# Kernel tuning notes

Measured on AMD Instinct MI355X. Metric: run time of the kernel, lower is better.

The kernel has to match this reference:

```python
import jax, jax.numpy as jnp
import numpy as np

B, T, D, H = 2, 2048, 1024, 16
DH = D // H


def setup_inputs() -> dict:
    key = jax.random.key(0)
    ks = jax.random.split(key, 11)
    s = 1.0 / np.sqrt(D)
    return {
        "q": jax.random.normal(ks[0], (B, T, D), jnp.float32),
        "k": jax.random.normal(ks[1], (B, T, D), jnp.float32),
        "v": jax.random.normal(ks[2], (B, T, D), jnp.float32),
        "wq_w": jax.random.normal(ks[3], (D, D), jnp.float32) * s,
        "wq_b": jnp.zeros((D,), jnp.float32),
        "wk_w": jax.random.normal(ks[4], (D, D), jnp.float32) * s,
        "wk_b": jnp.zeros((D,), jnp.float32),
        "wv_w": jax.random.normal(ks[5], (D, D), jnp.float32) * s,
        "wv_b": jnp.zeros((D,), jnp.float32),
        "wo_w": jax.random.normal(ks[6], (D, D), jnp.float32) * s,
        "wo_b": jnp.zeros((D,), jnp.float32),
    }


def reference(q, k, v, wq_w, wq_b, wk_w, wk_b, wv_w, wv_b, wo_w, wo_b):
    b, t, d = q.shape
    # Linear projections (torch Linear: x @ W^T + b)
    wq = (q @ wq_w.T + wq_b).reshape(b, t, H, DH)
    wk = (k @ wk_w.T + wk_b).reshape(b, t, H, DH)
    wv = (v @ wv_w.T + wv_b).reshape(b, t, H, DH)
    # scaled dot-product attention: [b,h,t,s]
    scores = jnp.einsum('bthd,bshd->bhts', wq, wk) / jnp.sqrt(jnp.float32(DH))
    probs = jax.nn.softmax(scores, axis=-1)
    attn = jnp.einsum('bhts,bshd->bthd', probs, wv)  # [b,t,h,dh]
    attn = attn.reshape(b, t, d)
    return attn @ wo_w.T + wo_b
```

## Files before the change

kernel.cpp:

```cpp
#include <hip/hip_runtime.h>
#include <hip/hip_bf16.h>
#include <stdint.h>

#define Bn  2
#define Tn  2048
#define Dn  1024
#define Hn  16
#define DHn 64
#define Mn  (Bn*Tn)

typedef __attribute__((ext_vector_type(8))) short short8;
typedef __attribute__((ext_vector_type(4))) short short4v;
typedef __attribute__((ext_vector_type(4))) float f32x4;

__device__ __forceinline__ f32x4 fzero4() { f32x4 z = {0.f, 0.f, 0.f, 0.f}; return z; }

#define TR16(dst, a32) asm volatile("ds_read_b64_tr_b16 %0, %1" : "=v"(dst) : "v"(a32))

__global__ void cvt4_kernel(const float* __restrict__ a0, const float* __restrict__ a1,
                            const float* __restrict__ a2, const float* __restrict__ a3,
                            __hip_bfloat16* __restrict__ o0, __hip_bfloat16* __restrict__ o1,
                            __hip_bfloat16* __restrict__ o2, __hip_bfloat16* __restrict__ o3, int n)
{
    const int i = (blockIdx.x * blockDim.x + threadIdx.x) * 8;
    if (i >= n) return;
    const float* in = blockIdx.y == 0 ? a0 : (blockIdx.y == 1 ? a1 : (blockIdx.y == 2 ? a2 : a3));
    __hip_bfloat16* out = blockIdx.y == 0 ? o0 : (blockIdx.y == 1 ? o1 : (blockIdx.y == 2 ? o2 : o3));
    float4 a = *(const float4*)(in + i);
    float4 b = *(const float4*)(in + i + 4);
    union { __hip_bfloat16 h[8]; short8 u; } tmp;
    tmp.h[0] = __float2bfloat16(a.x); tmp.h[1] = __float2bfloat16(a.y);
    tmp.h[2] = __float2bfloat16(a.z); tmp.h[3] = __float2bfloat16(a.w);
    tmp.h[4] = __float2bfloat16(b.x); tmp.h[5] = __float2bfloat16(b.y);
    tmp.h[6] = __float2bfloat16(b.z); tmp.h[7] = __float2bfloat16(b.w);
    *(short8*)(out + i) = tmp.u;
}

__global__ __launch_bounds__(256, 2)
void gemm_qkv_kernel(const float* __restrict__ qa, const float* __restrict__ ka,
                     const float* __restrict__ va,
                     const __hip_bfloat16* __restrict__ wq, const __hip_bfloat16* __restrict__ wk,
                     const __hip_bfloat16* __restrict__ wv,
                     const float* __restrict__ bq_, const float* __restrict__ bk_,
                     const float* __restrict__ bv_,
                     __hip_bfloat16* __restrict__ Qp, __hip_bfloat16* __restrict__ Kp,
                     __hip_bfloat16* __restrict__ Vp)
{
    __shared__ alignas(16) short As[2][128*32];
    __shared__ alignas(16) short Bs[2][128*32];
    const int grp = blockIdx.y >> 3;
    const float* A           = grp == 0 ? qa : (grp == 1 ? ka : va);
    const __hip_bfloat16* Bw = grp == 0 ? wq : (grp == 1 ? wk : wv);
    const float* bias        = grp == 0 ? bq_ : (grp == 1 ? bk_ : bv_);
    __hip_bfloat16* C        = grp == 0 ? Qp : (grp == 1 ? Kp : Vp);

    const int t = threadIdx.x, lane = t & 63, wave = t >> 6;
    const int wm = wave >> 1, wn = wave & 1;
    const int row0 = blockIdx.x * 128, col0 = (blockIdx.y & 7) * 128;

    f32x4 acc[4][4];
#pragma unroll
    for (int m = 0; m < 4; ++m)
#pragma unroll
        for (int n = 0; n < 4; ++n) acc[m][n] = fzero4();

    const int srow = wave*16 + (lane >> 2);
    const int skk  = (lane & 3) * 8;
    const int ldsb = wave * 1024 + (lane & 63) * 16;

    float4 ra[2][2];
    auto LOAD_A = [&](int k0) {
#pragma unroll
        for (int i = 0; i < 2; ++i) {
            const float* ap = A + (size_t)(row0 + i*64 + srow)*Dn + k0 + skk;
            ra[i][0] = *(const float4*)ap;
            ra[i][1] = *(const float4*)(ap + 4);
        }
    };
    auto WRITE_A = [&](int buf) {
#pragma unroll
        for (int i = 0; i < 2; ++i) {
            union { __hip_bfloat16 h[8]; short8 u; } w;
            w.h[0] = __float2bfloat16(ra[i][0].x); w.h[1] = __float2bfloat16(ra[i][0].y);
            w.h[2] = __float2bfloat16(ra[i][0].z); w.h[3] = __float2bfloat16(ra[i][0].w);
            w.h[4] = __float2bfloat16(ra[i][1].x); w.h[5] = __float2bfloat16(ra[i][1].y);
            w.h[6] = __float2bfloat16(ra[i][1].z); w.h[7] = __float2bfloat16(ra[i][1].w);
            *(short8*)((char*)As[buf] + i*4096 + ldsb) = w.u;
        }
    };
    auto STAGE_B = [&](int buf, int k0) {
#pragma unroll
        for (int i = 0; i < 2; ++i)
            __builtin_amdgcn_global_load_lds(
                (const __attribute__((address_space(1))) void*)(Bw + (size_t)(col0 + i*64 + srow)*Dn + k0 + skk),
                (__attribute__((address_space(3))) void*)((char*)Bs[buf] + i*4096 + wave*1024 + (lane&63)*16), 16, 0, 0);
    };

    LOAD_A(0);
    STAGE_B(0, 0);
    WRITE_A(0);
    __syncthreads();
    int cur = 0;
    for (int k0 = 0; k0 < Dn; k0 += 32) {
        const bool more = (k0 + 32 < Dn);
        if (more) { LOAD_A(k0 + 32); STAGE_B(cur ^ 1, k0 + 32); }
        short8 af[4], bf_[4];
#pragma unroll
        for (int m = 0; m < 4; ++m)
            af[m] = *(const short8*)((char*)As[cur] + (wm*64 + m*16 + (lane & 15))*64 + (lane >> 4)*16);
#pragma unroll
        for (int n = 0; n < 4; ++n)
            bf_[n] = *(const short8*)((char*)Bs[cur] + (wn*64 + n*16 + (lane & 15))*64 + (lane >> 4)*16);
        __builtin_amdgcn_s_setprio(1);
#pragma unroll
        for (int m = 0; m < 4; ++m)
#pragma unroll
            for (int n = 0; n < 4; ++n)
                acc[m][n] = __builtin_amdgcn_mfma_f32_16x16x32_bf16(af[m], bf_[n], acc[m][n], 0, 0, 0);
        __builtin_amdgcn_s_setprio(0);
        __builtin_amdgcn_sched_barrier(0);
        if (more) WRITE_A(cur ^ 1);
        __syncthreads();
        cur ^= 1;
    }

#pragma unroll
    for (int n = 0; n < 4; ++n) {
        const int col = col0 + wn*64 + n*16 + (lane & 15);
        const float bv = bias[col];
#pragma unroll
        for (int m = 0; m < 4; ++m) {
            const int rb_ = row0 + wm*64 + m*16 + (lane>>4)*4;
#pragma unroll
            for (int i = 0; i < 4; ++i)
                C[(size_t)(rb_+i)*Dn + col] = __float2bfloat16(acc[m][n][i] + bv);
        }
    }
}

__global__ __launch_bounds__(256, 2)
void gemm_out_kernel(const __hip_bfloat16* __restrict__ A,
                     const __hip_bfloat16* __restrict__ Bw,
                     const float* __restrict__ bias,
                     float* __restrict__ C)
{
    __shared__ alignas(16) short As[2][64*32];
    __shared__ alignas(16) short Bs[2][128*32];
    const int t = threadIdx.x, lane = t & 63, wave = t >> 6;
    const int wm = wave >> 1, wn = wave & 1;
    const int row0 = blockIdx.x * 64, col0 = blockIdx.y * 128;

    f32x4 acc[2][4];
#pragma unroll
    for (int m = 0; m < 2; ++m)
#pragma unroll
        for (int n = 0; n < 4; ++n) acc[m][n] = fzero4();

    const int srow = wave*16 + (lane >> 2);
    const int skk  = (lane & 3) * 8;
    const int ldsb = wave * 1024;

    auto STAGE = [&](int buf, int k0) {
        __builtin_amdgcn_global_load_lds(
            (const __attribute__((address_space(1))) void*)(A + (size_t)(row0 + srow)*Dn + k0 + skk),
            (__attribute__((address_space(3))) void*)((char*)As[buf] + ldsb), 16, 0, 0);
#pragma unroll
        for (int i = 0; i < 2; ++i)
            __builtin_amdgcn_global_load_lds(
                (const __attribute__((address_space(1))) void*)(Bw + (size_t)(col0 + i*64 + srow)*Dn + k0 + skk),
                (__attribute__((address_space(3))) void*)((char*)Bs[buf] + i*4096 + ldsb), 16, 0, 0);
    };

    STAGE(0, 0);
    __syncthreads();
    int cur = 0;
    for (int k0 = 0; k0 < Dn; k0 += 32) {
        if (k0 + 32 < Dn) STAGE(cur ^ 1, k0 + 32);
        short8 af[2], bf_[4];
#pragma unroll
        for (int m = 0; m < 2; ++m)
            af[m] = *(const short8*)((char*)As[cur] + (wm*32 + m*16 + (lane & 15))*64 + (lane >> 4)*16);
#pragma unroll
        for (int n = 0; n < 4; ++n)
            bf_[n] = *(const short8*)((char*)Bs[cur] + (wn*64 + n*16 + (lane & 15))*64 + (lane >> 4)*16);
        __builtin_amdgcn_s_setprio(1);
#pragma unroll
        for (int m = 0; m < 2; ++m)
#pragma unroll
            for (int n = 0; n < 4; ++n)
                acc[m][n] = __builtin_amdgcn_mfma_f32_16x16x32_bf16(af[m], bf_[n], acc[m][n], 0, 0, 0);
        __builtin_amdgcn_s_setprio(0);
        __syncthreads();
        cur ^= 1;
    }

#pragma unroll
    for (int n = 0; n < 4; ++n) {
        const int col = col0 + wn*64 + n*16 + (lane & 15);
        const float bv = bias[col];
#pragma unroll
        for (int m = 0; m < 2; ++m) {
            const int rb_ = row0 + wm*32 + m*16 + (lane>>4)*4;
#pragma unroll
            for (int i = 0; i < 4; ++i)
                C[(size_t)(rb_+i)*Dn + col] = acc[m][n][i] + bv;
        }
    }
}

#define VPL 1288

__global__ __launch_bounds__(256, 2)
void attn_kernel(const __hip_bfloat16* __restrict__ Q,
                 const __hip_bfloat16* __restrict__ K,
                 const __hip_bfloat16* __restrict__ V,
                 __hip_bfloat16* __restrict__ O)
{
    __shared__ alignas(16) short Vlds[2*2*4*VPL];
    const int t = threadIdx.x, lane = t & 63, wave = t >> 6;
    const int g = lane >> 4, c = lane & 15;
    const int pk = wave & 1, qh = wave >> 1;
    const int blk = (blockIdx.x & 7) * 64 + (blockIdx.x >> 3);
    const int qb = blk & 15;
    const int h  = (blk >> 4) & (Hn - 1);
    const int b  = blk >> 8;
    const size_t base = (size_t)b * Tn * Dn + (size_t)h * DHn;
    const int q0 = qb * 128 + qh * 64;
    const float cexp = 0.18033688011112042f;

    short8 bq[4][2];
#pragma unroll
    for (int qs = 0; qs < 4; ++qs) {
        const __hip_bfloat16* qp = Q + base + (size_t)(q0 + qs*16 + c) * Dn + g*8;
        bq[qs][0] = *(const short8*)qp;
        bq[qs][1] = *(const short8*)(qp + 32);
    }
    short8 ones;
#pragma unroll
    for (int i = 0; i < 8; ++i) ones[i] = (short)0x3F80;

    f32x4 o_[4][4];
#pragma unroll
    for (int qs = 0; qs < 4; ++qs)
#pragma unroll
        for (int d = 0; d < 4; ++d) o_[qs][d] = fzero4();
    float m_[4] = {-3e38f, -3e38f, -3e38f, -3e38f};
    f32x4 lacc[4] = {fzero4(), fzero4(), fzero4(), fzero4()};

    const int vrow = t >> 3;
    const int vd0  = ((t>>1)&3)*VPL + (vrow>>2)*80 + (vrow&3)*16 + (t&1)*8;
    const int vcol = (((t>>1)&3)*16 + (t&1)*8);
    const uint32_t vbase = (uint32_t)(uintptr_t)(void*)Vlds;
    const uint32_t atr = vbase + (uint32_t)(pk*10304 + g*160 + c*8);

    short8 akA[4][2], akB[4][2];
    {
        const __hip_bfloat16* kp = K + base + (size_t)(pk*64 + c) * Dn + g*8;
#pragma unroll
        for (int sub = 0; sub < 4; ++sub)
#pragma unroll
            for (int ks = 0; ks < 2; ++ks)
                akA[sub][ks] = *(const short8*)(kp + (size_t)sub*16*Dn + ks*32);
    }

    auto ITER = [&](const short8 (&ck)[4][2], short8 (&nk)[4][2], int it) {
        const int kv0 = it * 128;
        short8 cv[2][2];
#pragma unroll
        for (int p = 0; p < 2; ++p) {
            const __hip_bfloat16* vp = V + base + (size_t)(kv0 + p*64 + vrow) * Dn + vcol;
            cv[p][0] = *(const short8*)vp;
            cv[p][1] = *(const short8*)(vp + (size_t)32*Dn);
        }
        {
            const int kvn = (it < 15) ? kv0 + 128 + pk*64 : pk*64;
            const __hip_bfloat16* kp = K + base + (size_t)(kvn + c) * Dn + g*8;
#pragma unroll
            for (int sub = 0; sub < 4; ++sub)
#pragma unroll
                for (int ks = 0; ks < 2; ++ks)
                    nk[sub][ks] = *(const short8*)(kp + (size_t)sub*16*Dn + ks*32);
        }

        short8 pa[4][2];
#pragma unroll
        for (int qs = 0; qs < 4; ++qs) {
            f32x4 s_[4];
#pragma unroll
            for (int sub = 0; sub < 4; ++sub) s_[sub] = fzero4();
            __builtin_amdgcn_s_setprio(1);
#pragma unroll
            for (int sub = 0; sub < 4; ++sub)
#pragma unroll
                for (int ks = 0; ks < 2; ++ks)
                    s_[sub] = __builtin_amdgcn_mfma_f32_16x16x32_bf16(
                        ck[sub][ks], bq[qs][ks], s_[sub], 0, 0, 0);
            __builtin_amdgcn_s_setprio(0);

            float rm = s_[0][0];
#pragma unroll
            for (int sub = 0; sub < 4; ++sub)
#pragma unroll
                for (int i = 0; i < 4; ++i) rm = fmaxf(rm, s_[sub][i]);
            if (!__all((rm - m_[qs]) * cexp <= 8.0f)) {
                float gm = fmaxf(rm, __shfl_xor(rm, 16));
                gm = fmaxf(gm, __shfl_xor(gm, 32));
                const float mn = fmaxf(m_[qs], gm);
                const float sc = exp2f((m_[qs] - mn) * cexp);
                m_[qs] = mn;
#pragma unroll
                for (int i = 0; i < 4; ++i) lacc[qs][i] *= sc;
#pragma unroll
                for (int d = 0; d < 4; ++d)
#pragma unroll
                    for (int i = 0; i < 4; ++i) o_[qs][d][i] *= sc;
            }
            const float mn = m_[qs];
#pragma unroll
            for (int kc = 0; kc < 2; ++kc)
#pragma unroll
                for (int hf = 0; hf < 2; ++hf)
#pragma unroll
                    for (int i = 0; i < 4; ++i) {
                        const float p = exp2f((s_[kc*2+hf][i] - mn) * cexp);
                        union { __hip_bfloat16 hb; short u; } cvp;
                        cvp.hb = __float2bfloat16(p);
                        pa[qs][kc][hf*4 + i] = cvp.u;
                    }
            lacc[qs] = __builtin_amdgcn_mfma_f32_16x16x32_bf16(ones, pa[qs][0], lacc[qs], 0, 0, 0);
            lacc[qs] = __builtin_amdgcn_mfma_f32_16x16x32_bf16(ones, pa[qs][1], lacc[qs], 0, 0, 0);
        }

        short* vb = Vlds + (it & 1) * 10304;
#pragma unroll
        for (int p = 0; p < 2; ++p) {
            *(short8*)(vb + p*5152 + vd0)       = cv[p][0];
            *(short8*)(vb + p*5152 + vd0 + 640) = cv[p][1];
        }
        asm volatile("s_waitcnt lgkmcnt(0)" ::: "memory");
        __builtin_amdgcn_s_barrier();
        __builtin_amdgcn_sched_barrier(0);

        const uint32_t atrb = atr + (uint32_t)((it & 1) * 20608u);
        short4v tv[4][2][2];
#pragma unroll
        for (int d = 0; d < 4; ++d)
#pragma unroll
            for (int kc = 0; kc < 2; ++kc) {
                const uint32_t a = atrb + (uint32_t)(d*2576 + kc*1280);
                TR16(tv[d][kc][0], a);
                TR16(tv[d][kc][1], a + 640);
            }
#pragma unroll
        for (int d = 0; d < 4; ++d) {
            if (d == 0)      asm volatile("s_waitcnt lgkmcnt(12)" ::: "memory");
            else if (d == 1) asm volatile("s_waitcnt lgkmcnt(8)" ::: "memory");
            else if (d == 2) asm volatile("s_waitcnt lgkmcnt(4)" ::: "memory");
            else             asm volatile("s_waitcnt lgkmcnt(0)" ::: "memory");
            __builtin_amdgcn_sched_barrier(0);
            const short8 av0 = __builtin_shufflevector(tv[d][0][0], tv[d][0][1], 0,1,2,3,4,5,6,7);
            const short8 av1 = __builtin_shufflevector(tv[d][1][0], tv[d][1][1], 0,1,2,3,4,5,6,7);
            __builtin_amdgcn_s_setprio(1);
#pragma unroll
            for (int qs = 0; qs < 4; ++qs) {
                o_[qs][d] = __builtin_amdgcn_mfma_f32_16x16x32_bf16(av0, pa[qs][0], o_[qs][d], 0, 0, 0);
                o_[qs][d] = __builtin_amdgcn_mfma_f32_16x16x32_bf16(av1, pa[qs][1], o_[qs][d], 0, 0, 0);
            }
            __builtin_amdgcn_s_setprio(0);
        }
    };

    for (int j = 0; j < 8; ++j) {
        ITER(akA, akB, 2*j);
        ITER(akB, akA, 2*j + 1);
    }

    __syncthreads();
    float* cbase = (float*)Vlds;
    if (pk == 1) {
        float* cb = cbase + qh * 4608;
#pragma unroll
        for (int qs = 0; qs < 4; ++qs)
#pragma unroll
            for (int d = 0; d < 4; ++d)
                *(f32x4*)(cb + ((qs*4 + d)*64 + lane)*4) = o_[qs][d];
#pragma unroll
        for (int qs = 0; qs < 4; ++qs) {
            cb[4096 + qs*64 + lane] = m_[qs];
            cb[4352 + qs*64 + lane] = lacc[qs][0];
        }
    }
    __syncthreads();
    if (pk == 0) {
        float* cb = cbase + qh * 4608;
#pragma unroll
        for (int qs = 0; qs < 4; ++qs) {
            const float m1 = cb[4096 + qs*64 + lane];
            const float l1 = cb[4352 + qs*64 + lane];
            const float mN = fmaxf(m_[qs], m1);
            const float sc0 = exp2f((m_[qs] - mN) * cexp);
            const float sc1 = exp2f((m1 - mN) * cexp);
            const float inv = 1.f / (lacc[qs][0]*sc0 + l1*sc1);
            __hip_bfloat16* op = O + base + (size_t)(q0 + qs*16 + c) * Dn + g*4;
#pragma unroll
            for (int d = 0; d < 4; ++d) {
                const f32x4 o1 = *(const f32x4*)(cb + ((qs*4 + d)*64 + lane)*4);
                union { __hip_bfloat16 hb[4]; ushort4 u4; } w;
#pragma unroll
                for (int i = 0; i < 4; ++i)
                    w.hb[i] = __float2bfloat16((o_[qs][d][i]*sc0 + o1[i]*sc1) * inv);
                *(ushort4*)(op + d*16) = w.u4;
            }
        }
    }
}

extern "C" void kernel_launch(void* const* d_in, const int* in_sizes, int n_in,
                              void* d_out, int out_size, void* d_ws, size_t ws_size,
                              hipStream_t stream)
{
    (void)in_sizes; (void)n_in; (void)out_size; (void)ws_size;
    const float* q    = (const float*)d_in[0];
    const float* k    = (const float*)d_in[1];
    const float* v    = (const float*)d_in[2];
    const float* wq_w = (const float*)d_in[3];
    const float* wq_b = (const float*)d_in[4];
    const float* wk_w = (const float*)d_in[5];
    const float* wk_b = (const float*)d_in[6];
    const float* wv_w = (const float*)d_in[7];
    const float* wv_b = (const float*)d_in[8];
    const float* wo_w = (const float*)d_in[9];
    const float* wo_b = (const float*)d_in[10];

    char* ws = (char*)d_ws;
    const size_t S1 = (size_t)Mn * Dn * 2;
    const size_t W  = (size_t)Dn * Dn * 2;
    __hip_bfloat16* wqb = (__hip_bfloat16*)(ws);
    __hip_bfloat16* wkb = (__hip_bfloat16*)(ws + W);
    __hip_bfloat16* wvb = (__hip_bfloat16*)(ws + 2*W);
    __hip_bfloat16* wob = (__hip_bfloat16*)(ws + 3*W);
    __hip_bfloat16* Qp  = (__hip_bfloat16*)(ws + 4*W);
    __hip_bfloat16* Kp  = (__hip_bfloat16*)(ws + 4*W + S1);
    __hip_bfloat16* Vp  = (__hip_bfloat16*)(ws + 4*W + 2*S1);
    __hip_bfloat16* Ap  = (__hip_bfloat16*)(ws + 4*W + 3*S1);

    const int nW = Dn * Dn;
    cvt4_kernel<<<dim3(nW/2048, 4), 256, 0, stream>>>(wq_w, wk_w, wv_w, wo_w,
                                                      wqb, wkb, wvb, wob, nW);

    gemm_qkv_kernel<<<dim3(Mn/128, 24), 256, 0, stream>>>(
        q, k, v, wqb, wkb, wvb, wq_b, wk_b, wv_b, Qp, Kp, Vp);

    attn_kernel<<<Bn*Hn*(Tn/128), 256, 0, stream>>>(Qp, Kp, Vp, Ap);

    gemm_out_kernel<<<dim3(Mn/64, Dn/128), 256, 0, stream>>>(Ap, wob, wo_b, (float*)d_out);
}
```

Baseline: 136.5 us.

## Split attention KV range four ways per block with single-buffered V tile

Each attention block now handles 64 query rows, and its four waves each process a quarter of the key/value sequence (split-K). Partial softmax states are then merged through LDS in a two-level reduction. The grid doubles to 1024 blocks and V staging becomes single-buffered with an extra barrier before writes. Launch bounds for attention and the QKV GEMM are raised to 3 waves-per-EU occupancy, aiming for more parallelism and better latency hiding. In exchange there are more merge barriers, redundant Q loads per block, and possible register spills under the tighter bound.

New measurement: 445.5 us. 226% more time.

```diff
diff --git a/kernel.cpp b/kernel.cpp
--- a/kernel.cpp
+++ b/kernel.cpp
@@ -36,7 +36,7 @@
     *(short8*)(out + i) = tmp.u;
 }
 
-__global__ __launch_bounds__(256, 2)
+__global__ __launch_bounds__(256, 3)
 void gemm_qkv_kernel(const float* __restrict__ qa, const float* __restrict__ ka,
                      const float* __restrict__ va,
                      const __hip_bfloat16* __restrict__ wq, const __hip_bfloat16* __restrict__ wk,
@@ -208,24 +208,24 @@
     }
 }
 
-#define VPL 1288
-
-__global__ __launch_bounds__(256, 2)
+#define VPL   1288
+#define TILEB 10304
+
+__global__ __launch_bounds__(256, 3)
 void attn_kernel(const __hip_bfloat16* __restrict__ Q,
                  const __hip_bfloat16* __restrict__ K,
                  const __hip_bfloat16* __restrict__ V,
                  __hip_bfloat16* __restrict__ O)
 {
-    __shared__ alignas(16) short Vlds[2*2*4*VPL];
+    __shared__ alignas(16) short Vlds[4*4*VPL];
     const int t = threadIdx.x, lane = t & 63, wave = t >> 6;
     const int g = lane >> 4, c = lane & 15;
-    const int pk = wave & 1, qh = wave >> 1;
-    const int blk = (blockIdx.x & 7) * 64 + (blockIdx.x >> 3);
-    const int qb = blk & 15;
-    const int h  = (blk >> 4) & (Hn - 1);
-    const int b  = blk >> 8;
+    const int blk = (blockIdx.x & 7) * 128 + (blockIdx.x >> 3);
+    const int qb = blk & 31;
+    const int bh = blk >> 5;
+    const int h  = bh & (Hn - 1), b = bh >> 4;
     const size_t base = (size_t)b * Tn * Dn + (size_t)h * DHn;
-    const int q0 = qb * 128 + qh * 64;
+    const int q0 = qb * 64;
     const float cexp = 0.18033688011112042f;
 
     short8 bq[4][2];
@@ -247,15 +247,14 @@
     float m_[4] = {-3e38f, -3e38f, -3e38f, -3e38f};
     f32x4 lacc[4] = {fzero4(), fzero4(), fzero4(), fzero4()};
 
-    const int vrow = t >> 3;
-    const int vd0  = ((t>>1)&3)*VPL + (vrow>>2)*80 + (vrow&3)*16 + (t&1)*8;
-    const int vcol = (((t>>1)&3)*16 + (t&1)*8);
+    const int srow8 = t >> 3, scol = t & 7;
+    const int wconst = (scol>>1)*2576 + (srow8>>2)*160 + (srow8&3)*32 + (scol&1)*16;
     const uint32_t vbase = (uint32_t)(uintptr_t)(void*)Vlds;
-    const uint32_t atr = vbase + (uint32_t)(pk*10304 + g*160 + c*8);
+    const uint32_t atr = vbase + (uint32_t)(wave*TILEB + g*160 + c*8);
 
     short8 akA[4][2], akB[4][2];
     {
-        const __hip_bfloat16* kp = K + base + (size_t)(pk*64 + c) * Dn + g*8;
+        const __hip_bfloat16* kp = K + base + (size_t)(wave*64 + c) * Dn + g*8;
 #pragma unroll
         for (int sub = 0; sub < 4; ++sub)
 #pragma unroll
@@ -264,16 +263,14 @@
     }
 
     auto ITER = [&](const short8 (&ck)[4][2], short8 (&nk)[4][2], int it) {
-        const int kv0 = it * 128;
-        short8 cv[2][2];
-#pragma unroll
-        for (int p = 0; p < 2; ++p) {
-            const __hip_bfloat16* vp = V + base + (size_t)(kv0 + p*64 + vrow) * Dn + vcol;
-            cv[p][0] = *(const short8*)vp;
-            cv[p][1] = *(const short8*)(vp + (size_t)32*Dn);
-        }
+        const int kv0 = it * 256;
+        short8 cv[8];
+        const __hip_bfloat16* vp = V + base + (size_t)(kv0 + srow8) * Dn + scol*8;
+#pragma unroll
+        for (int j = 0; j < 8; ++j)
+            cv[j] = *(const short8*)(vp + (size_t)(32*j) * Dn);
         {
-            const int kvn = (it < 15) ? kv0 + 128 + pk*64 : pk*64;
+            const int kvn = (it < 7) ? kv0 + 256 + wave*64 : wave*64;
             const __hip_bfloat16* kp = K + base + (size_t)(kvn + c) * Dn + g*8;
 #pragma unroll
             for (int sub = 0; sub < 4; ++sub)
@@ -331,23 +328,20 @@
             lacc[qs] = __builtin_amdgcn_mfma_f32_16x16x32_bf16(ones, pa[qs][1], lacc[qs], 0, 0, 0);
         }
 
-        short* vb = Vlds + (it & 1) * 10304;
-#pragma unroll
-        for (int p = 0; p < 2; ++p) {
-            *(short8*)(vb + p*5152 + vd0)       = cv[p][0];
-            *(short8*)(vb + p*5152 + vd0 + 640) = cv[p][1];
-        }
+        __builtin_amdgcn_s_barrier();
+#pragma unroll
+        for (int j = 0; j < 8; ++j)
+            *(short8*)((char*)Vlds + (j>>1)*TILEB + (j&1)*1280 + wconst) = cv[j];
         asm volatile("s_waitcnt lgkmcnt(0)" ::: "memory");
         __builtin_amdgcn_s_barrier();
         __builtin_amdgcn_sched_barrier(0);
 
-        const uint32_t atrb = atr + (uint32_t)((it & 1) * 20608u);
         short4v tv[4][2][2];
 #pragma unroll
         for (int d = 0; d < 4; ++d)
 #pragma unroll
             for (int kc = 0; kc < 2; ++kc) {
-                const uint32_t a = atrb + (uint32_t)(d*2576 + kc*1280);
+                const uint32_t a = atr + (uint32_t)(d*2576 + kc*1280);
                 TR16(tv[d][kc][0], a);
                 TR16(tv[d][kc][1], a + 640);
             }
@@ -370,45 +364,63 @@
         }
     };
 
-    for (int j = 0; j < 8; ++j) {
+    for (int j = 0; j < 4; ++j) {
         ITER(akA, akB, 2*j);
         ITER(akB, akA, 2*j + 1);
     }
 
     __syncthreads();
-    float* cbase = (float*)Vlds;
-    if (pk == 1) {
-        float* cb = cbase + qh * 4608;
-#pragma unroll
-        for (int qs = 0; qs < 4; ++qs)
+    float* cb = (float*)Vlds;
+    auto DUMP = [&](int slot) {
+        float* p = cb + slot * 4608;
+#pragma unroll
+        for (int qs = 0; qs < 4; ++qs) {
 #pragma unroll
             for (int d = 0; d < 4; ++d)
-                *(f32x4*)(cb + ((qs*4 + d)*64 + lane)*4) = o_[qs][d];
+                *(f32x4*)(p + ((qs*4 + d)*64 + lane)*4) = o_[qs][d];
+            p[4096 + qs*64 + lane] = m_[qs];
+            p[4352 + qs*64 + lane] = lacc[qs][0];
+        }
+    };
+    auto MERGE = [&](int slot) {
+        float* p = cb + slot * 4608;
 #pragma unroll
         for (int qs = 0; qs < 4; ++qs) {
-            cb[4096 + qs*64 + lane] = m_[qs];
-            cb[4352 + qs*64 + lane] = lacc[qs][0];
-        }
-    }
-    __syncthreads();
-    if (pk == 0) {
-        float* cb = cbase + qh * 4608;
-#pragma unroll
-        for (int qs = 0; qs < 4; ++qs) {
-            const float m1 = cb[4096 + qs*64 + lane];
-            const float l1 = cb[4352 + qs*64 + lane];
+            const float m1 = p[4096 + qs*64 + lane];
+            const float l1 = p[4352 + qs*64 + lane];
             const float mN = fmaxf(m_[qs], m1);
             const float sc0 = exp2f((m_[qs] - mN) * cexp);
             const float sc1 = exp2f((m1 - mN) * cexp);
-            const float inv = 1.f / (lacc[qs][0]*sc0 + l1*sc1);
+            m_[qs] = mN;
+            lacc[qs][0] = lacc[qs][0]*sc0 + l1*sc1;
+#pragma unroll
+            for (int d = 0; d < 4; ++d) {
+                const f32x4 o1 = *(const f32x4*)(p + ((qs*4 + d)*64 + lane)*4);
+#pragma unroll
+                for (int i = 0; i < 4; ++i)
+                    o_[qs][d][i] = o_[qs][d][i]*sc0 + o1[i]*sc1;
+            }
+        }
+    };
+    if (wave == 1) DUMP(0);
+    if (wave == 3) DUMP(1);
+    __syncthreads();
+    if (wave == 0) MERGE(0);
+    if (wave == 2) MERGE(1);
+    __syncthreads();
+    if (wave == 2) DUMP(0);
+    __syncthreads();
+    if (wave == 0) {
+        MERGE(0);
+#pragma unroll
+        for (int qs = 0; qs < 4; ++qs) {
+            const float inv = 1.f / lacc[qs][0];
             __hip_bfloat16* op = O + base + (size_t)(q0 + qs*16 + c) * Dn + g*4;
 #pragma unroll
             for (int d = 0; d < 4; ++d) {
-                const f32x4 o1 = *(const f32x4*)(cb + ((qs*4 + d)*64 + lane)*4);
                 union { __hip_bfloat16 hb[4]; ushort4 u4; } w;
 #pragma unroll
-                for (int i = 0; i < 4; ++i)
-                    w.hb[i] = __float2bfloat16((o_[qs][d][i]*sc0 + o1[i]*sc1) * inv);
+                for (int i = 0; i < 4; ++i) w.hb[i] = __float2bfloat16(o_[qs][d][i] * inv);
                 *(ushort4*)(op + d*16) = w.u4;
             }
         }
@@ -451,7 +463,7 @@
     gemm_qkv_kernel<<<dim3(Mn/128, 24), 256, 0, stream>>>(
         q, k, v, wqb, wkb, wvb, wq_b, wk_b, wv_b, Qp, Kp, Vp);
 
-    attn_kernel<<<Bn*Hn*(Tn/128), 256, 0, stream>>>(Qp, Kp, Vp, Ap);
+    attn_kernel<<<Bn*Hn*(Tn/64), 256, 0, stream>>>(Qp, Kp, Vp, Ap);
 
     gemm_out_kernel<<<dim3(Mn/64, Dn/128), 256, 0, stream>>>(Ap, wob, wo_b, (float*)d_out);
 }
```
